# Optimization experiments

Hardware: AMD Instinct MI355X
Metric: run time of the kernel (lower is better)

## Reference

```python
import jax, jax.numpy as jnp
import numpy as np

EPS = 1e-5
LOSS_WEIGHT = 0.3
IGNORE_INDEX = -100


def rmsnorm(x, w):
    # x: (B,S,D), w: (D,)
    var = jnp.mean(x * x, axis=-1, keepdims=True)
    return x * jax.lax.rsqrt(var + EPS) * w


def cross_entropy(logits, targets):
    # logits: (B,T,V), targets: (B,T) int; ignore_index=-100, mean reduction
    logp = jax.nn.log_softmax(logits, axis=-1)
    valid = targets != IGNORE_INDEX
    safe_t = jnp.where(valid, targets, 0)
    nll = -jnp.take_along_axis(logp, safe_t[..., None], axis=-1)[..., 0]
    nll = jnp.where(valid, nll, 0.0)
    return jnp.sum(nll) / jnp.maximum(jnp.sum(valid), 1)


def setup_inputs() -> dict:
    key = jax.random.key(0)
    ks = jax.random.split(key, 5)
    B, S, D, V, H = 1, 2048, 1024, 50257, 3
    hidden = jax.random.normal(ks[0], (B, S, D), dtype=jnp.float32)
    targets = jax.random.randint(ks[1], (B, S), 0, V, dtype=jnp.int64)
    emb_w = jax.random.normal(ks[2], (V, D), dtype=jnp.float32) * 0.02
    main_norm_w = jnp.ones((D,), dtype=jnp.float32)
    aux_proj_w = jax.random.normal(ks[3], (H - 1, D, D), dtype=jnp.float32) * 0.02
    aux_norm_w = jnp.ones((H - 1, D), dtype=jnp.float32)
    aux_out_w = jax.random.normal(ks[4], (H - 1, V, D), dtype=jnp.float32) * 0.02
    return {"hidden": hidden, "targets": targets, "emb_w": emb_w,
            "main_norm_w": main_norm_w, "aux_proj_w": aux_proj_w,
            "aux_norm_w": aux_norm_w, "aux_out_w": aux_out_w}


def reference(hidden, targets, emb_w, main_norm_w, aux_proj_w, aux_norm_w, aux_out_w):
    # Main head: norm -> tied vocab projection
    main_logits = jnp.einsum('bsd,vd->bsv', rmsnorm(hidden, main_norm_w), emb_w)
    main_loss = cross_entropy(main_logits[:, :-1, :], targets[:, 1:])

    # Auxiliary heads predict t+2, t+3, ...
    n_aux = aux_proj_w.shape[0]
    aux_losses = []
    for i in range(n_aux):
        k = i + 2
        h = jnp.einsum('bsd,ed->bse', hidden, aux_proj_w[i])  # d_model -> d_model
        logits = jnp.einsum('bsd,vd->bsv', rmsnorm(h, aux_norm_w[i]), aux_out_w[i])
        aux_losses.append(cross_entropy(logits[:, :-k, :], targets[:, k:]))
    total_aux = sum(aux_losses) / len(aux_losses) if aux_losses else jnp.float32(0.0)
    loss = main_loss + LOSS_WEIGHT * total_aux
    return main_logits, loss
```

## Files before the change

### kernel.cpp

```cpp
#include <hip/hip_runtime.h>
#include <hip/hip_bf16.h>


typedef __hip_bfloat16 bf16;
typedef __attribute__((ext_vector_type(8))) short bf16x8;
typedef __attribute__((ext_vector_type(4))) float f32x4;

typedef const __attribute__((address_space(1))) void* gptr_t;
typedef __attribute__((address_space(3))) void* lptr_t;

#define S_LEN   2048
#define DMODEL  1024
#define VOCAB   50257
#define VPAD    50304
#define NTILES  393

__device__ __forceinline__ void gload_lds16(const void* g, void* l) {
  __builtin_amdgcn_global_load_lds((gptr_t)g, (lptr_t)l, 16, 0, 0);
}

__global__ __launch_bounds__(256) void k_cvt(const float* __restrict__ src,
                                             bf16* __restrict__ dst,
                                             long rows_src, long rows_pad) {
  const long total4 = rows_pad << 8;
  for (long i = (long)blockIdx.x * 256 + threadIdx.x; i < total4;
       i += (long)gridDim.x * 256) {
    const long e = i << 2;
    const long row = e >> 10;
    alignas(8) bf16 o[4];
    if (row < rows_src) {
      const float4 v = *(const float4*)(src + e);
      o[0] = __float2bfloat16(v.x); o[1] = __float2bfloat16(v.y);
      o[2] = __float2bfloat16(v.z); o[3] = __float2bfloat16(v.w);
    } else {
      o[0] = o[1] = o[2] = o[3] = __float2bfloat16(0.f);
    }
    *(uint2*)(dst + e) = *(const uint2*)o;
  }
}

__global__ __launch_bounds__(256) void k_rms(const float* __restrict__ x,
                                             const float* __restrict__ w,
                                             bf16* __restrict__ xn) {
  const int row = blockIdx.x;
  const int t = threadIdx.x;
  const float4 v = ((const float4*)(x + (size_t)row * DMODEL))[t];
  float ss = v.x*v.x + v.y*v.y + v.z*v.z + v.w*v.w;
  #pragma unroll
  for (int d = 1; d < 64; d <<= 1) ss += __shfl_xor(ss, d, 64);
  __shared__ float red[4];
  if ((t & 63) == 0) red[t >> 6] = ss;
  __syncthreads();
  const float tot = red[0] + red[1] + red[2] + red[3];
  const float scale = rsqrtf(tot * (1.f / DMODEL) + 1e-5f);
  const float4 wv = ((const float4*)w)[t];
  alignas(8) bf16 o[4];
  o[0] = __float2bfloat16(v.x * scale * wv.x);
  o[1] = __float2bfloat16(v.y * scale * wv.y);
  o[2] = __float2bfloat16(v.z * scale * wv.z);
  o[3] = __float2bfloat16(v.w * scale * wv.w);
  *(uint2*)(xn + (size_t)row * DMODEL + t * 4) = *(const uint2*)o;
}

template<bool WRITE_OUT, bool DO_CE>
__global__ __launch_bounds__(256, 2)
void k_gemm(const bf16* __restrict__ A, const bf16* __restrict__ B,
            float* __restrict__ C, long ldc, int Nvalid,
            const int* __restrict__ targets, int shift,
            float* __restrict__ pmax, float* __restrict__ psum,
            float* __restrict__ ptgt, int ntiles) {
  constexpr int K = DMODEL;
  __shared__ bf16 As[128 * 32];
  __shared__ bf16 Bs[128 * 32];

  const int t = threadIdx.x;
  const int bn = blockIdx.x, bm = blockIdx.y;
  const int w = t >> 6, l = t & 63, g = l >> 4, q = l & 15;
  const int wr = w >> 1, wc = w & 1;

  f32x4 acc[4][4];
  #pragma unroll
  for (int i = 0; i < 4; ++i)
    #pragma unroll
    for (int j = 0; j < 4; ++j)
      #pragma unroll
      for (int r = 0; r < 4; ++r) acc[i][j][r] = 0.f;

  char* lA0 = (char*)As + w * 1024;
  char* lA1 = (char*)As + 4096 + w * 1024;
  char* lB0 = (char*)Bs + w * 1024;
  char* lB1 = (char*)Bs + 4096 + w * 1024;
  const char* gA0 = (const char*)(A + (size_t)(bm * 128 + (t >> 2)) * K) + (t & 3) * 16;
  const char* gA1 = gA0 + (size_t)64 * K * 2;
  const char* gB0 = (const char*)(B + (size_t)(bn * 128 + (t >> 2)) * K) + (t & 3) * 16;
  const char* gB1 = gB0 + (size_t)64 * K * 2;

  for (int k0 = 0; k0 < K; k0 += 32) {
    const int kb = k0 * 2;
    gload_lds16(gA0 + kb, lA0);
    gload_lds16(gA1 + kb, lA1);
    gload_lds16(gB0 + kb, lB0);
    gload_lds16(gB1 + kb, lB1);
    __syncthreads();
    bf16x8 a[4], b[4];
    #pragma unroll
    for (int mi = 0; mi < 4; ++mi)
      a[mi] = *(const bf16x8*)&As[(wr * 64 + mi * 16 + q) * 32 + g * 8];
    #pragma unroll
    for (int ni = 0; ni < 4; ++ni)
      b[ni] = *(const bf16x8*)&Bs[(wc * 64 + ni * 16 + q) * 32 + g * 8];
    #pragma unroll
    for (int mi = 0; mi < 4; ++mi)
      #pragma unroll
      for (int ni = 0; ni < 4; ++ni)
        acc[mi][ni] = __builtin_amdgcn_mfma_f32_16x16x32_bf16(a[mi], b[ni], acc[mi][ni], 0, 0, 0);
    __syncthreads();
  }

  if constexpr (WRITE_OUT) {
    #pragma unroll
    for (int mi = 0; mi < 4; ++mi) {
      #pragma unroll
      for (int r = 0; r < 4; ++r) {
        const long row = bm * 128 + wr * 64 + mi * 16 + g * 4 + r;
        #pragma unroll
        for (int ni = 0; ni < 4; ++ni) {
          const int col = bn * 128 + wc * 64 + ni * 16 + q;
          if (col < Nvalid) C[row * ldc + col] = acc[mi][ni][r];
        }
      }
    }
  }

  if constexpr (DO_CE) {
    __shared__ float lds_m[128][2];
    __shared__ float lds_s[128][2];
    __shared__ int lds_tgt[128];
    if (t < 128) {
      const int rowg = bm * 128 + t;
      lds_tgt[t] = (rowg < S_LEN - shift) ? targets[rowg + shift] : -1;
    }
    __syncthreads();
    #pragma unroll
    for (int mi = 0; mi < 4; ++mi) {
      #pragma unroll
      for (int r = 0; r < 4; ++r) {
        const int rl = wr * 64 + mi * 16 + g * 4 + r;
        const int tgt = lds_tgt[rl];
        float v[4];
        #pragma unroll
        for (int ni = 0; ni < 4; ++ni) {
          const int n = bn * 128 + wc * 64 + ni * 16 + q;
          const float a = acc[mi][ni][r];
          if (n == tgt) ptgt[bm * 128 + rl] = a;
          v[ni] = (n < Nvalid) ? a : -1e30f;
        }
        float m = fmaxf(fmaxf(v[0], v[1]), fmaxf(v[2], v[3]));
        #pragma unroll
        for (int d = 1; d < 16; d <<= 1) m = fmaxf(m, __shfl_xor(m, d, 64));
        float s = 0.f;
        #pragma unroll
        for (int ni = 0; ni < 4; ++ni) s += __expf(v[ni] - m);
        #pragma unroll
        for (int d = 1; d < 16; d <<= 1) s += __shfl_xor(s, d, 64);
        if (q == 0) { lds_m[rl][wc] = m; lds_s[rl][wc] = s; }
      }
    }
    __syncthreads();
    if (t < 128) {
      const float m0 = lds_m[t][0], m1 = lds_m[t][1];
      const float s0 = lds_s[t][0], s1 = lds_s[t][1];
      const float M = fmaxf(m0, m1);
      const float Ssum = s0 * __expf(m0 - M) + s1 * __expf(m1 - M);
      const size_t idx = (size_t)(bm * 128 + t) * ntiles + bn;
      pmax[idx] = M;
      psum[idx] = Ssum;
    }
  }
}

__global__ __launch_bounds__(64) void k_combine(const float* __restrict__ pmax,
                                                const float* __restrict__ psum,
                                                const float* __restrict__ ptgt,
                                                float* __restrict__ nll,
                                                int ntiles, int nv) {
  const int r = blockIdx.x;
  const int l = threadIdx.x;
  float M = -1e30f, Ssum = 0.f;
  for (int tl = l; tl < ntiles; tl += 64) {
    const float m = pmax[(size_t)r * ntiles + tl];
    const float s = psum[(size_t)r * ntiles + tl];
    const float nM = fmaxf(M, m);
    Ssum = Ssum * __expf(M - nM) + s * __expf(m - nM);
    M = nM;
  }
  #pragma unroll
  for (int d = 1; d < 64; d <<= 1) {
    const float m2 = __shfl_xor(M, d, 64);
    const float s2 = __shfl_xor(Ssum, d, 64);
    const float nM = fmaxf(M, m2);
    Ssum = Ssum * __expf(M - nM) + s2 * __expf(m2 - nM);
    M = nM;
  }
  if (l == 0) nll[r] = (r < nv) ? (M + logf(Ssum) - ptgt[r]) : 0.f;
}

__global__ __launch_bounds__(256) void k_loss(const float* __restrict__ nll,
                                              float* __restrict__ out) {
  __shared__ float sh[256];
  const int t = threadIdx.x;
  float sums[3];
  #pragma unroll
  for (int h = 0; h < 3; ++h) {
    const int nv = 2047 - h;
    float s = 0.f;
    for (int r = t; r < nv; r += 256) s += nll[h * 2048 + r];
    sh[t] = s; __syncthreads();
    for (int off = 128; off > 0; off >>= 1) {
      if (t < off) sh[t] += sh[t + off];
      __syncthreads();
    }
    sums[h] = sh[0]; __syncthreads();
  }
  if (t == 0)
    out[0] = sums[0] / 2047.f + 0.3f * 0.5f * (sums[1] / 2046.f + sums[2] / 2045.f);
}

extern "C" void kernel_launch(void* const* d_in, const int* in_sizes, int n_in,
                              void* d_out, int out_size, void* d_ws, size_t ws_size,
                              hipStream_t stream) {
  const float* hidden      = (const float*)d_in[0];
  const int*   targets     = (const int*)d_in[1];
  const float* emb_w       = (const float*)d_in[2];
  const float* main_norm_w = (const float*)d_in[3];
  const float* aux_proj_w  = (const float*)d_in[4];
  const float* aux_norm_w  = (const float*)d_in[5];
  const float* aux_out_w   = (const float*)d_in[6];
  float* out = (float*)d_out;

  char* ws = (char*)d_ws;
  bf16*  Wb    = (bf16*)(ws);
  bf16*  hb    = (bf16*)(ws + 103022592);
  bf16*  projb = (bf16*)(ws + 107216896);
  bf16*  xn    = (bf16*)(ws + 111411200);
  float* hbuf  = (float*)(ws + 115605504);
  float* pmax  = (float*)(ws + 123994112);
  float* psum  = (float*)(ws + 127213568);
  float* ptgt  = (float*)(ws + 130433024);
  float* nll   = (float*)(ws + 130441216);

  k_cvt<<<2048, 256, 0, stream>>>(hidden, hb, 2048, 2048);
  k_cvt<<<2048, 256, 0, stream>>>(aux_proj_w, projb, 2048, 2048);
  k_rms<<<2048, 256, 0, stream>>>(hidden, main_norm_w, xn);

  k_cvt<<<2048, 256, 0, stream>>>(emb_w, Wb, VOCAB, VPAD);
  k_gemm<true, true><<<dim3(NTILES, 16), 256, 0, stream>>>(
      xn, Wb, out, VOCAB, VOCAB, targets, 1, pmax, psum, ptgt, NTILES);
  k_combine<<<2048, 64, 0, stream>>>(pmax, psum, ptgt, nll, NTILES, 2047);

  for (int i = 0; i < 2; ++i) {
    k_cvt<<<2048, 256, 0, stream>>>(aux_out_w + (size_t)i * VOCAB * DMODEL, Wb, VOCAB, VPAD);
    k_gemm<true, false><<<dim3(8, 16), 256, 0, stream>>>(
        hb, projb + (size_t)i * DMODEL * DMODEL, hbuf, DMODEL, DMODEL,
        nullptr, 0, nullptr, nullptr, nullptr, 0);
    k_rms<<<2048, 256, 0, stream>>>(hbuf, aux_norm_w + (size_t)i * DMODEL, xn);
    k_gemm<false, true><<<dim3(NTILES, 16), 256, 0, stream>>>(
        xn, Wb, nullptr, 0, VOCAB, targets, i + 2, pmax, psum, ptgt, NTILES);
    k_combine<<<2048, 64, 0, stream>>>(pmax, psum, ptgt, nll + (i + 1) * 2048, NTILES, 2048 - (i + 2));
  }

  k_loss<<<1, 256, 0, stream>>>(nll, out + (size_t)S_LEN * VOCAB);
}
```

Before: 1.218 ms.

## Use 256x256 double-buffered GEMM tile for vocab projections with fused CE

Adds a new 512-thread GEMM kernel with 256x256 output tiles, a K-step of 64, and double-buffered LDS staging through direct global-to-LDS loads. It interleaves prefetch with MFMA phases using explicit waitcnt, barriers and setprio, and swaps the grid so blockIdx.x walks M tiles, keeping the same weight tile shared across neighbouring blocks. The larger tile halves the number of vocab tiles and partial softmax entries, which cuts operand reloads and combine work. In exchange it uses about 140KB of LDS per block and many more accumulator registers, which may lower occupancy.

Result: no change. 1.240 ms (+1.8%).

```diff
diff --git a/kernel.cpp b/kernel.cpp
--- a/kernel.cpp
+++ b/kernel.cpp
@@ -12,8 +12,8 @@
 #define S_LEN   2048
 #define DMODEL  1024
 #define VOCAB   50257
-#define VPAD    50304
-#define NTILES  393
+#define VPAD2   50432
+#define NT256   197
 
 __device__ __forceinline__ void gload_lds16(const void* g, void* l) {
   __builtin_amdgcn_global_load_lds((gptr_t)g, (lptr_t)l, 16, 0, 0);
@@ -63,12 +63,184 @@
 }
 
 template<bool WRITE_OUT, bool DO_CE>
+__global__ __launch_bounds__(512, 2)
+void k_gemm256(const bf16* __restrict__ A, const bf16* __restrict__ B,
+               float* __restrict__ C, long ldc, int Nvalid,
+               const int* __restrict__ targets, int shift,
+               float* __restrict__ pmax, float* __restrict__ psum,
+               float* __restrict__ ptgt, int ntiles) {
+  __shared__ char lds[131072 + 9216];
+
+  const int t = threadIdx.x;
+  const int w = t >> 6, l = t & 63;
+  const int g = l >> 4, q = l & 15;
+  const int wr = w >> 2, wc = w & 3;
+  const int bm = blockIdx.x, bn = blockIdx.y;
+
+  f32x4 acc[8][4];
+  #pragma unroll
+  for (int i = 0; i < 8; ++i)
+    #pragma unroll
+    for (int j = 0; j < 4; ++j)
+      #pragma unroll
+      for (int r = 0; r < 4; ++r) acc[i][j][r] = 0.f;
+
+  const int srow = (l >> 2);
+  const int scol = (l & 3) * 8;
+  const bf16* gA0 = A + (size_t)(bm * 256 + (w * 2 + 0) * 16 + srow) * DMODEL + scol;
+  const bf16* gA1 = A + (size_t)(bm * 256 + (w * 2 + 1) * 16 + srow) * DMODEL + scol;
+  const bf16* gB0 = B + (size_t)(bn * 256 + (w * 2 + 0) * 16 + srow) * DMODEL + scol;
+  const bf16* gB1 = B + (size_t)(bn * 256 + (w * 2 + 1) * 16 + srow) * DMODEL + scol;
+
+  auto stage = [&](int buf, int h, int tt) {
+    const int kbase = tt * 64 + (h >> 1) * 32;
+    char* lb = lds + buf * 65536 + (h >> 1) * 32768 + (h & 1) * 16384 + (w * 2) * 1024;
+    if (h & 1) {
+      gload_lds16(gB0 + kbase, lb);
+      gload_lds16(gB1 + kbase, lb + 1024);
+    } else {
+      gload_lds16(gA0 + kbase, lb);
+      gload_lds16(gA1 + kbase, lb + 1024);
+    }
+  };
+
+  const int laneoff = q * 64 + g * 16;
+  auto lda = [&](int buf, int kk, int mi) {
+    return *(const bf16x8*)(lds + buf * 65536 + kk * 32768 + (wr * 8 + mi) * 1024 + laneoff);
+  };
+  auto ldb = [&](int buf, int kk, int ni) {
+    return *(const bf16x8*)(lds + buf * 65536 + kk * 32768 + 16384 + (wc * 4 + ni) * 1024 + laneoff);
+  };
+
+  stage(0, 0, 0); stage(0, 1, 0); stage(0, 2, 0); stage(0, 3, 0);
+  asm volatile("s_waitcnt vmcnt(4)" ::: "memory");
+  __builtin_amdgcn_s_barrier();
+  __builtin_amdgcn_sched_barrier(0);
+
+  #define PHASE_MFMA(MH, KK)                                                     \
+    __builtin_amdgcn_s_barrier();                                                \
+    __builtin_amdgcn_sched_barrier(0);                                           \
+    __builtin_amdgcn_s_setprio(1);                                               \
+    _Pragma("unroll")                                                            \
+    for (int mi = 0; mi < 4; ++mi)                                               \
+      _Pragma("unroll")                                                          \
+      for (int ni = 0; ni < 4; ++ni)                                             \
+        acc[(MH)*4 + mi][ni] = __builtin_amdgcn_mfma_f32_16x16x32_bf16(          \
+            a[mi], b[ni], acc[(MH)*4 + mi][ni], 0, 0, 0);                        \
+    __builtin_amdgcn_s_setprio(0);                                               \
+    __builtin_amdgcn_sched_barrier(0);
+
+  for (int tt = 0; tt < 16; ++tt) {
+    const int buf = tt & 1, nbuf = buf ^ 1;
+    const bool pre = tt < 15;
+    bf16x8 a[4], b[4];
+
+    #pragma unroll
+    for (int mi = 0; mi < 4; ++mi) a[mi] = lda(buf, 0, mi);
+    #pragma unroll
+    for (int ni = 0; ni < 4; ++ni) b[ni] = ldb(buf, 0, ni);
+    if (pre) stage(nbuf, 0, tt + 1);
+    PHASE_MFMA(0, 0)
+    __builtin_amdgcn_s_barrier();
+    __builtin_amdgcn_sched_barrier(0);
+
+    #pragma unroll
+    for (int mi = 0; mi < 4; ++mi) a[mi] = lda(buf, 0, 4 + mi);
+    if (pre) stage(nbuf, 1, tt + 1);
+    PHASE_MFMA(1, 0)
+    if (pre) asm volatile("s_waitcnt vmcnt(4)" ::: "memory");
+    else     asm volatile("s_waitcnt vmcnt(0)" ::: "memory");
+    __builtin_amdgcn_s_barrier();
+    __builtin_amdgcn_sched_barrier(0);
+
+    #pragma unroll
+    for (int mi = 0; mi < 4; ++mi) a[mi] = lda(buf, 1, mi);
+    #pragma unroll
+    for (int ni = 0; ni < 4; ++ni) b[ni] = ldb(buf, 1, ni);
+    if (pre) stage(nbuf, 2, tt + 1);
+    PHASE_MFMA(0, 1)
+    __builtin_amdgcn_s_barrier();
+    __builtin_amdgcn_sched_barrier(0);
+
+    #pragma unroll
+    for (int mi = 0; mi < 4; ++mi) a[mi] = lda(buf, 1, 4 + mi);
+    if (pre) stage(nbuf, 3, tt + 1);
+    PHASE_MFMA(1, 1)
+    if (pre) asm volatile("s_waitcnt vmcnt(4)" ::: "memory");
+    __builtin_amdgcn_s_barrier();
+    __builtin_amdgcn_sched_barrier(0);
+  }
+  #undef PHASE_MFMA
+
+  if constexpr (WRITE_OUT) {
+    #pragma unroll
+    for (int mi = 0; mi < 8; ++mi) {
+      #pragma unroll
+      for (int r = 0; r < 4; ++r) {
+        const long row = bm * 256 + wr * 128 + mi * 16 + g * 4 + r;
+        #pragma unroll
+        for (int ni = 0; ni < 4; ++ni) {
+          const int col = bn * 256 + wc * 64 + ni * 16 + q;
+          if (col < Nvalid) C[row * ldc + col] = acc[mi][ni][r];
+        }
+      }
+    }
+  }
+
+  if constexpr (DO_CE) {
+    float* lds_m = (float*)(lds + 131072);
+    float* lds_s = lds_m + 1024;
+    int* lds_tgt = (int*)(lds_s + 1024);
+    if (t < 256) {
+      const int rowg = bm * 256 + t;
+      lds_tgt[t] = (rowg < S_LEN - shift) ? targets[rowg + shift] : -1;
+    }
+    __syncthreads();
+    #pragma unroll
+    for (int mi = 0; mi < 8; ++mi) {
+      #pragma unroll
+      for (int r = 0; r < 4; ++r) {
+        const int rl = wr * 128 + mi * 16 + g * 4 + r;
+        const int tgt = lds_tgt[rl];
+        float v[4];
+        #pragma unroll
+        for (int ni = 0; ni < 4; ++ni) {
+          const int n = bn * 256 + wc * 64 + ni * 16 + q;
+          const float av = acc[mi][ni][r];
+          if (n == tgt) ptgt[bm * 256 + rl] = av;
+          v[ni] = (n < Nvalid) ? av : -1e30f;
+        }
+        float m = fmaxf(fmaxf(v[0], v[1]), fmaxf(v[2], v[3]));
+        #pragma unroll
+        for (int d = 1; d < 16; d <<= 1) m = fmaxf(m, __shfl_xor(m, d, 64));
+        float s = 0.f;
+        #pragma unroll
+        for (int ni = 0; ni < 4; ++ni) s += __expf(v[ni] - m);
+        #pragma unroll
+        for (int d = 1; d < 16; d <<= 1) s += __shfl_xor(s, d, 64);
+        if (q == 0) { lds_m[rl * 4 + wc] = m; lds_s[rl * 4 + wc] = s; }
+      }
+    }
+    __syncthreads();
+    if (t < 256) {
+      float M = lds_m[t * 4 + 0], Ssum = lds_s[t * 4 + 0];
+      #pragma unroll
+      for (int c = 1; c < 4; ++c) {
+        const float m2 = lds_m[t * 4 + c], s2 = lds_s[t * 4 + c];
+        const float nM = fmaxf(M, m2);
+        Ssum = Ssum * __expf(M - nM) + s2 * __expf(m2 - nM);
+        M = nM;
+      }
+      const size_t idx = (size_t)(bm * 256 + t) * ntiles + bn;
+      pmax[idx] = M;
+      psum[idx] = Ssum;
+    }
+  }
+}
+
 __global__ __launch_bounds__(256, 2)
 void k_gemm(const bf16* __restrict__ A, const bf16* __restrict__ B,
-            float* __restrict__ C, long ldc, int Nvalid,
-            const int* __restrict__ targets, int shift,
-            float* __restrict__ pmax, float* __restrict__ psum,
-            float* __restrict__ ptgt, int ntiles) {
+            float* __restrict__ C, long ldc, int Nvalid) {
   constexpr int K = DMODEL;
   __shared__ bf16 As[128 * 32];
   __shared__ bf16 Bs[128 * 32];
@@ -117,64 +289,16 @@
     __syncthreads();
   }
 
-  if constexpr (WRITE_OUT) {
-    #pragma unroll
-    for (int mi = 0; mi < 4; ++mi) {
-      #pragma unroll
-      for (int r = 0; r < 4; ++r) {
-        const long row = bm * 128 + wr * 64 + mi * 16 + g * 4 + r;
-        #pragma unroll
-        for (int ni = 0; ni < 4; ++ni) {
-          const int col = bn * 128 + wc * 64 + ni * 16 + q;
-          if (col < Nvalid) C[row * ldc + col] = acc[mi][ni][r];
-        }
+  #pragma unroll
+  for (int mi = 0; mi < 4; ++mi) {
+    #pragma unroll
+    for (int r = 0; r < 4; ++r) {
+      const long row = bm * 128 + wr * 64 + mi * 16 + g * 4 + r;
+      #pragma unroll
+      for (int ni = 0; ni < 4; ++ni) {
+        const int col = bn * 128 + wc * 64 + ni * 16 + q;
+        if (col < Nvalid) C[row * ldc + col] = acc[mi][ni][r];
       }
-    }
-  }
-
-  if constexpr (DO_CE) {
-    __shared__ float lds_m[128][2];
-    __shared__ float lds_s[128][2];
-    __shared__ int lds_tgt[128];
-    if (t < 128) {
-      const int rowg = bm * 128 + t;
-      lds_tgt[t] = (rowg < S_LEN - shift) ? targets[rowg + shift] : -1;
-    }
-    __syncthreads();
-    #pragma unroll
-    for (int mi = 0; mi < 4; ++mi) {
-      #pragma unroll
-      for (int r = 0; r < 4; ++r) {
-        const int rl = wr * 64 + mi * 16 + g * 4 + r;
-        const int tgt = lds_tgt[rl];
-        float v[4];
-        #pragma unroll
-        for (int ni = 0; ni < 4; ++ni) {
-          const int n = bn * 128 + wc * 64 + ni * 16 + q;
-          const float a = acc[mi][ni][r];
-          if (n == tgt) ptgt[bm * 128 + rl] = a;
-          v[ni] = (n < Nvalid) ? a : -1e30f;
-        }
-        float m = fmaxf(fmaxf(v[0], v[1]), fmaxf(v[2], v[3]));
-        #pragma unroll
-        for (int d = 1; d < 16; d <<= 1) m = fmaxf(m, __shfl_xor(m, d, 64));
-        float s = 0.f;
-        #pragma unroll
-        for (int ni = 0; ni < 4; ++ni) s += __expf(v[ni] - m);
-        #pragma unroll
-        for (int d = 1; d < 16; d <<= 1) s += __shfl_xor(s, d, 64);
-        if (q == 0) { lds_m[rl][wc] = m; lds_s[rl][wc] = s; }
-      }
-    }
-    __syncthreads();
-    if (t < 128) {
-      const float m0 = lds_m[t][0], m1 = lds_m[t][1];
-      const float s0 = lds_s[t][0], s1 = lds_s[t][1];
-      const float M = fmaxf(m0, m1);
-      const float Ssum = s0 * __expf(m0 - M) + s1 * __expf(m1 - M);
-      const size_t idx = (size_t)(bm * 128 + t) * ntiles + bn;
-      pmax[idx] = M;
-      psum[idx] = Ssum;
     }
   }
 }
@@ -240,33 +364,32 @@
 
   char* ws = (char*)d_ws;
   bf16*  Wb    = (bf16*)(ws);
-  bf16*  hb    = (bf16*)(ws + 103022592);
-  bf16*  projb = (bf16*)(ws + 107216896);
-  bf16*  xn    = (bf16*)(ws + 111411200);
-  float* hbuf  = (float*)(ws + 115605504);
-  float* pmax  = (float*)(ws + 123994112);
-  float* psum  = (float*)(ws + 127213568);
-  float* ptgt  = (float*)(ws + 130433024);
-  float* nll   = (float*)(ws + 130441216);
+  bf16*  hb    = (bf16*)(ws + 103284736);
+  bf16*  xn    = (bf16*)(ws + 107479040);
+  bf16*  projb = (bf16*)(ws + 111673344);
+  float* hbuf  = (float*)(ws + 115867648);
+  float* pmax  = (float*)(ws + 124256256);
+  float* psum  = (float*)(ws + 125870080);
+  float* ptgt  = (float*)(ws + 127483904);
+  float* nll   = (float*)(ws + 127492096);
 
   k_cvt<<<2048, 256, 0, stream>>>(hidden, hb, 2048, 2048);
   k_cvt<<<2048, 256, 0, stream>>>(aux_proj_w, projb, 2048, 2048);
   k_rms<<<2048, 256, 0, stream>>>(hidden, main_norm_w, xn);
 
-  k_cvt<<<2048, 256, 0, stream>>>(emb_w, Wb, VOCAB, VPAD);
-  k_gemm<true, true><<<dim3(NTILES, 16), 256, 0, stream>>>(
-      xn, Wb, out, VOCAB, VOCAB, targets, 1, pmax, psum, ptgt, NTILES);
-  k_combine<<<2048, 64, 0, stream>>>(pmax, psum, ptgt, nll, NTILES, 2047);
+  k_cvt<<<2048, 256, 0, stream>>>(emb_w, Wb, VOCAB, VPAD2);
+  k_gemm256<true, true><<<dim3(8, NT256), 512, 0, stream>>>(
+      xn, Wb, out, VOCAB, VOCAB, targets, 1, pmax, psum, ptgt, NT256);
+  k_combine<<<2048, 64, 0, stream>>>(pmax, psum, ptgt, nll, NT256, 2047);
 
   for (int i = 0; i < 2; ++i) {
-    k_cvt<<<2048, 256, 0, stream>>>(aux_out_w + (size_t)i * VOCAB * DMODEL, Wb, VOCAB, VPAD);
-    k_gemm<true, false><<<dim3(8, 16), 256, 0, stream>>>(
-        hb, projb + (size_t)i * DMODEL * DMODEL, hbuf, DMODEL, DMODEL,
-        nullptr, 0, nullptr, nullptr, nullptr, 0);
+    k_cvt<<<2048, 256, 0, stream>>>(aux_out_w + (size_t)i * VOCAB * DMODEL, Wb, VOCAB, VPAD2);
+    k_gemm<<<dim3(8, 16), 256, 0, stream>>>(
+        hb, projb + (size_t)i * DMODEL * DMODEL, hbuf, DMODEL, DMODEL);
     k_rms<<<2048, 256, 0, stream>>>(hbuf, aux_norm_w + (size_t)i * DMODEL, xn);
-    k_gemm<false, true><<<dim3(NTILES, 16), 256, 0, stream>>>(
-        xn, Wb, nullptr, 0, VOCAB, targets, i + 2, pmax, psum, ptgt, NTILES);
-    k_combine<<<2048, 64, 0, stream>>>(pmax, psum, ptgt, nll + (i + 1) * 2048, NTILES, 2048 - (i + 2));
+    k_gemm256<false, true><<<dim3(8, NT256), 512, 0, stream>>>(
+        xn, Wb, nullptr, 0, VOCAB, targets, i + 2, pmax, psum, ptgt, NT256);
+    k_combine<<<2048, 64, 0, stream>>>(pmax, psum, ptgt, nll + (i + 1) * 2048, NT256, 2048 - (i + 2));
   }
 
   k_loss<<<1, 256, 0, stream>>>(nll, out + (size_t)S_LEN * VOCAB);
```

## Add swizzled LDS, grouped tile rasterization and MFMA priority to vocab GEMM

Applied to the files above, without the earlier changes.

Introduces a dedicated vocab-projection GEMM kernel with a 1D grid remapped so that 8 column-groups times 16 row tiles are scheduled together, improving L2 reuse of the weight tiles. It XOR-swizzles the LDS layout on both the global-to-LDS load and the fragment reads to cut bank conflicts, and raises wave priority around the MFMA block. The vocabulary padding grows to 400 tiles so the remap divides evenly, which adds a few extra padded tiles of work and conversion. The small projection GEMM is split into a simpler kernel without the CE template.

Result: faster. 1.146 ms (-5.9%).

```diff
diff --git a/kernel.cpp b/kernel.cpp
--- a/kernel.cpp
+++ b/kernel.cpp
@@ -12,8 +12,8 @@
 #define S_LEN   2048
 #define DMODEL  1024
 #define VOCAB   50257
-#define VPAD    50304
-#define NTILES  393
+#define VPAD2   51200
+#define NT128   400
 
 __device__ __forceinline__ void gload_lds16(const void* g, void* l) {
   __builtin_amdgcn_global_load_lds((gptr_t)g, (lptr_t)l, 16, 0, 0);
@@ -62,13 +62,131 @@
   *(uint2*)(xn + (size_t)row * DMODEL + t * 4) = *(const uint2*)o;
 }
 
-template<bool WRITE_OUT, bool DO_CE>
+template<bool WRITE_OUT>
+__global__ __launch_bounds__(256, 2)
+void k_gemm128(const bf16* __restrict__ A, const bf16* __restrict__ B,
+               float* __restrict__ C, long ldc, int Nvalid,
+               const int* __restrict__ targets, int shift,
+               float* __restrict__ pmax, float* __restrict__ psum,
+               float* __restrict__ ptgt, int ntiles) {
+  constexpr int K = DMODEL;
+  __shared__ bf16 As[128 * 32];
+  __shared__ bf16 Bs[128 * 32];
+  __shared__ float lds_m[128][2];
+  __shared__ float lds_s[128][2];
+  __shared__ int lds_tgt[128];
+
+  const int t = threadIdx.x;
+  const int w = t >> 6, l = t & 63, g = l >> 4, q = l & 15;
+  const int wr = w >> 1, wc = w & 1;
+  const int id = blockIdx.x;
+  const int bm = (id >> 3) & 15;
+  const int bn = (id & 7) * 50 + (id >> 7);
+
+  f32x4 acc[4][4];
+  #pragma unroll
+  for (int i = 0; i < 4; ++i)
+    #pragma unroll
+    for (int j = 0; j < 4; ++j)
+      #pragma unroll
+      for (int r = 0; r < 4; ++r) acc[i][j][r] = 0.f;
+
+  char* lA0 = (char*)As + w * 1024;
+  char* lA1 = (char*)As + 4096 + w * 1024;
+  char* lB0 = (char*)Bs + w * 1024;
+  char* lB1 = (char*)Bs + 4096 + w * 1024;
+  const int scol = ((t & 3) * 16) ^ (((t >> 5) & 1) * 32);
+  const char* gA0 = (const char*)(A + (size_t)(bm * 128 + (t >> 2)) * K) + scol;
+  const char* gA1 = gA0 + (size_t)64 * K * 2;
+  const char* gB0 = (const char*)(B + (size_t)(bn * 128 + (t >> 2)) * K) + scol;
+  const char* gB1 = gB0 + (size_t)64 * K * 2;
+
+  const int laneoff = (q * 64 + g * 16) ^ (((q >> 3) & 1) << 5);
+  const char* rdA = (const char*)As + wr * 4096 + laneoff;
+  const char* rdB = (const char*)Bs + wc * 4096 + laneoff;
+
+  for (int k0 = 0; k0 < K; k0 += 32) {
+    const int kb = k0 * 2;
+    gload_lds16(gA0 + kb, lA0);
+    gload_lds16(gA1 + kb, lA1);
+    gload_lds16(gB0 + kb, lB0);
+    gload_lds16(gB1 + kb, lB1);
+    __syncthreads();
+    bf16x8 a[4], b[4];
+    #pragma unroll
+    for (int mi = 0; mi < 4; ++mi) a[mi] = *(const bf16x8*)(rdA + mi * 1024);
+    #pragma unroll
+    for (int ni = 0; ni < 4; ++ni) b[ni] = *(const bf16x8*)(rdB + ni * 1024);
+    __builtin_amdgcn_s_setprio(1);
+    #pragma unroll
+    for (int mi = 0; mi < 4; ++mi)
+      #pragma unroll
+      for (int ni = 0; ni < 4; ++ni)
+        acc[mi][ni] = __builtin_amdgcn_mfma_f32_16x16x32_bf16(a[mi], b[ni], acc[mi][ni], 0, 0, 0);
+    __builtin_amdgcn_s_setprio(0);
+    __syncthreads();
+  }
+
+  if constexpr (WRITE_OUT) {
+    #pragma unroll
+    for (int mi = 0; mi < 4; ++mi) {
+      #pragma unroll
+      for (int r = 0; r < 4; ++r) {
+        const long row = bm * 128 + wr * 64 + mi * 16 + g * 4 + r;
+        #pragma unroll
+        for (int ni = 0; ni < 4; ++ni) {
+          const int col = bn * 128 + wc * 64 + ni * 16 + q;
+          if (col < Nvalid) C[row * ldc + col] = acc[mi][ni][r];
+        }
+      }
+    }
+  }
+
+  if (t < 128) {
+    const int rowg = bm * 128 + t;
+    lds_tgt[t] = (rowg < S_LEN - shift) ? targets[rowg + shift] : -1;
+  }
+  __syncthreads();
+  #pragma unroll
+  for (int mi = 0; mi < 4; ++mi) {
+    #pragma unroll
+    for (int r = 0; r < 4; ++r) {
+      const int rl = wr * 64 + mi * 16 + g * 4 + r;
+      const int tgt = lds_tgt[rl];
+      float v[4];
+      #pragma unroll
+      for (int ni = 0; ni < 4; ++ni) {
+        const int n = bn * 128 + wc * 64 + ni * 16 + q;
+        const float av = acc[mi][ni][r];
+        if (n == tgt) ptgt[bm * 128 + rl] = av;
+        v[ni] = (n < Nvalid) ? av : -1e30f;
+      }
+      float m = fmaxf(fmaxf(v[0], v[1]), fmaxf(v[2], v[3]));
+      #pragma unroll
+      for (int d = 1; d < 16; d <<= 1) m = fmaxf(m, __shfl_xor(m, d, 64));
+      float s = 0.f;
+      #pragma unroll
+      for (int ni = 0; ni < 4; ++ni) s += __expf(v[ni] - m);
+      #pragma unroll
+      for (int d = 1; d < 16; d <<= 1) s += __shfl_xor(s, d, 64);
+      if (q == 0) { lds_m[rl][wc] = m; lds_s[rl][wc] = s; }
+    }
+  }
+  __syncthreads();
+  if (t < 128) {
+    const float m0 = lds_m[t][0], m1 = lds_m[t][1];
+    const float s0 = lds_s[t][0], s1 = lds_s[t][1];
+    const float M = fmaxf(m0, m1);
+    const float Ssum = s0 * __expf(m0 - M) + s1 * __expf(m1 - M);
+    const size_t idx = (size_t)(bm * 128 + t) * ntiles + bn;
+    pmax[idx] = M;
+    psum[idx] = Ssum;
+  }
+}
+
 __global__ __launch_bounds__(256, 2)
 void k_gemm(const bf16* __restrict__ A, const bf16* __restrict__ B,
-            float* __restrict__ C, long ldc, int Nvalid,
-            const int* __restrict__ targets, int shift,
-            float* __restrict__ pmax, float* __restrict__ psum,
-            float* __restrict__ ptgt, int ntiles) {
+            float* __restrict__ C, long ldc, int Nvalid) {
   constexpr int K = DMODEL;
   __shared__ bf16 As[128 * 32];
   __shared__ bf16 Bs[128 * 32];
@@ -117,64 +235,16 @@
     __syncthreads();
   }
 
-  if constexpr (WRITE_OUT) {
-    #pragma unroll
-    for (int mi = 0; mi < 4; ++mi) {
-      #pragma unroll
-      for (int r = 0; r < 4; ++r) {
-        const long row = bm * 128 + wr * 64 + mi * 16 + g * 4 + r;
-        #pragma unroll
-        for (int ni = 0; ni < 4; ++ni) {
-          const int col = bn * 128 + wc * 64 + ni * 16 + q;
-          if (col < Nvalid) C[row * ldc + col] = acc[mi][ni][r];
-        }
+  #pragma unroll
+  for (int mi = 0; mi < 4; ++mi) {
+    #pragma unroll
+    for (int r = 0; r < 4; ++r) {
+      const long row = bm * 128 + wr * 64 + mi * 16 + g * 4 + r;
+      #pragma unroll
+      for (int ni = 0; ni < 4; ++ni) {
+        const int col = bn * 128 + wc * 64 + ni * 16 + q;
+        if (col < Nvalid) C[row * ldc + col] = acc[mi][ni][r];
       }
-    }
-  }
-
-  if constexpr (DO_CE) {
-    __shared__ float lds_m[128][2];
-    __shared__ float lds_s[128][2];
-    __shared__ int lds_tgt[128];
-    if (t < 128) {
-      const int rowg = bm * 128 + t;
-      lds_tgt[t] = (rowg < S_LEN - shift) ? targets[rowg + shift] : -1;
-    }
-    __syncthreads();
-    #pragma unroll
-    for (int mi = 0; mi < 4; ++mi) {
-      #pragma unroll
-      for (int r = 0; r < 4; ++r) {
-        const int rl = wr * 64 + mi * 16 + g * 4 + r;
-        const int tgt = lds_tgt[rl];
-        float v[4];
-        #pragma unroll
-        for (int ni = 0; ni < 4; ++ni) {
-          const int n = bn * 128 + wc * 64 + ni * 16 + q;
-          const float a = acc[mi][ni][r];
-          if (n == tgt) ptgt[bm * 128 + rl] = a;
-          v[ni] = (n < Nvalid) ? a : -1e30f;
-        }
-        float m = fmaxf(fmaxf(v[0], v[1]), fmaxf(v[2], v[3]));
-        #pragma unroll
-        for (int d = 1; d < 16; d <<= 1) m = fmaxf(m, __shfl_xor(m, d, 64));
-        float s = 0.f;
-        #pragma unroll
-        for (int ni = 0; ni < 4; ++ni) s += __expf(v[ni] - m);
-        #pragma unroll
-        for (int d = 1; d < 16; d <<= 1) s += __shfl_xor(s, d, 64);
-        if (q == 0) { lds_m[rl][wc] = m; lds_s[rl][wc] = s; }
-      }
-    }
-    __syncthreads();
-    if (t < 128) {
-      const float m0 = lds_m[t][0], m1 = lds_m[t][1];
-      const float s0 = lds_s[t][0], s1 = lds_s[t][1];
-      const float M = fmaxf(m0, m1);
-      const float Ssum = s0 * __expf(m0 - M) + s1 * __expf(m1 - M);
-      const size_t idx = (size_t)(bm * 128 + t) * ntiles + bn;
-      pmax[idx] = M;
-      psum[idx] = Ssum;
     }
   }
 }
@@ -240,33 +310,32 @@
 
   char* ws = (char*)d_ws;
   bf16*  Wb    = (bf16*)(ws);
-  bf16*  hb    = (bf16*)(ws + 103022592);
-  bf16*  projb = (bf16*)(ws + 107216896);
-  bf16*  xn    = (bf16*)(ws + 111411200);
-  float* hbuf  = (float*)(ws + 115605504);
-  float* pmax  = (float*)(ws + 123994112);
-  float* psum  = (float*)(ws + 127213568);
-  float* ptgt  = (float*)(ws + 130433024);
-  float* nll   = (float*)(ws + 130441216);
+  bf16*  hb    = (bf16*)(ws + 104857600);
+  bf16*  xn    = (bf16*)(ws + 109051904);
+  bf16*  projb = (bf16*)(ws + 113246208);
+  float* hbuf  = (float*)(ws + 117440512);
+  float* pmax  = (float*)(ws + 125829120);
+  float* psum  = (float*)(ws + 129105920);
+  float* ptgt  = (float*)(ws + 132382720);
+  float* nll   = (float*)(ws + 132390912);
 
   k_cvt<<<2048, 256, 0, stream>>>(hidden, hb, 2048, 2048);
   k_cvt<<<2048, 256, 0, stream>>>(aux_proj_w, projb, 2048, 2048);
   k_rms<<<2048, 256, 0, stream>>>(hidden, main_norm_w, xn);
 
-  k_cvt<<<2048, 256, 0, stream>>>(emb_w, Wb, VOCAB, VPAD);
-  k_gemm<true, true><<<dim3(NTILES, 16), 256, 0, stream>>>(
-      xn, Wb, out, VOCAB, VOCAB, targets, 1, pmax, psum, ptgt, NTILES);
-  k_combine<<<2048, 64, 0, stream>>>(pmax, psum, ptgt, nll, NTILES, 2047);
+  k_cvt<<<2048, 256, 0, stream>>>(emb_w, Wb, VOCAB, VPAD2);
+  k_gemm128<true><<<6400, 256, 0, stream>>>(
+      xn, Wb, out, VOCAB, VOCAB, targets, 1, pmax, psum, ptgt, NT128);
+  k_combine<<<2048, 64, 0, stream>>>(pmax, psum, ptgt, nll, NT128, 2047);
 
   for (int i = 0; i < 2; ++i) {
-    k_cvt<<<2048, 256, 0, stream>>>(aux_out_w + (size_t)i * VOCAB * DMODEL, Wb, VOCAB, VPAD);
-    k_gemm<true, false><<<dim3(8, 16), 256, 0, stream>>>(
-        hb, projb + (size_t)i * DMODEL * DMODEL, hbuf, DMODEL, DMODEL,
-        nullptr, 0, nullptr, nullptr, nullptr, 0);
+    k_cvt<<<2048, 256, 0, stream>>>(aux_out_w + (size_t)i * VOCAB * DMODEL, Wb, VOCAB, VPAD2);
+    k_gemm<<<dim3(8, 16), 256, 0, stream>>>(
+        hb, projb + (size_t)i * DMODEL * DMODEL, hbuf, DMODEL, DMODEL);
     k_rms<<<2048, 256, 0, stream>>>(hbuf, aux_norm_w + (size_t)i * DMODEL, xn);
-    k_gemm<false, true><<<dim3(NTILES, 16), 256, 0, stream>>>(
-        xn, Wb, nullptr, 0, VOCAB, targets, i + 2, pmax, psum, ptgt, NTILES);
-    k_combine<<<2048, 64, 0, stream>>>(pmax, psum, ptgt, nll + (i + 1) * 2048, NTILES, 2048 - (i + 2));
+    k_gemm128<false><<<6400, 256, 0, stream>>>(
+        xn, Wb, nullptr, 0, VOCAB, targets, i + 2, pmax, psum, ptgt, NT128);
+    k_combine<<<2048, 64, 0, stream>>>(pmax, psum, ptgt, nll + (i + 1) * 2048, NT128, 2048 - (i + 2));
   }
 
   k_loss<<<1, 256, 0, stream>>>(nll, out + (size_t)S_LEN * VOCAB);
```
